# Performance work log

Measured on AMD Instinct MI355X. Metric: run time of the kernel, lower is better.

Reference implementation:

```python
import jax, jax.numpy as jnp
import numpy as np

N, E, D, G, L = 100000, 1600000, 128, 64, 3


def _layernorm(h, g, b, eps=1e-5):
    mu = jnp.mean(h, axis=-1, keepdims=True)
    var = jnp.var(h, axis=-1, keepdims=True)
    return (h - mu) * jax.lax.rsqrt(var + eps) * g + b


def setup_inputs() -> dict:
    key = jax.random.key(0)
    ks = jax.random.split(key, 10)
    s = 1.0 / np.sqrt(D)
    return {
        "x": jax.random.normal(ks[0], (N, D), dtype=jnp.float32),
        "edge_index": jax.random.randint(ks[1], (2, E), 0, N, dtype=jnp.int64),
        "batch": jnp.sort(jax.random.randint(ks[2], (N,), 0, G, dtype=jnp.int64)),
        "fc_w": jax.random.normal(ks[3], (D, D), dtype=jnp.float32) * s,
        "fc_b": jnp.zeros((D,), dtype=jnp.float32),
        "w_self": jax.random.normal(ks[4], (L, D, D), dtype=jnp.float32) * s,
        "w_neigh": jax.random.normal(ks[5], (L, D, D), dtype=jnp.float32) * s,
        "conv_b": jnp.zeros((L, D), dtype=jnp.float32),
        "ln_g": jnp.ones((L, D), dtype=jnp.float32),
        "ln_b": jnp.zeros((L, D), dtype=jnp.float32),
    }


def reference(x, edge_index, batch, fc_w, fc_b, w_self, w_neigh, conv_b, ln_g, ln_b):
    src, dst = edge_index[0], edge_index[1]
    # in-degree for mean aggregation (clamped to avoid div-by-zero)
    deg = jax.ops.segment_sum(jnp.ones((E,), dtype=x.dtype), dst, num_segments=N)
    deg = jnp.maximum(deg, 1.0)[:, None]  # [N,1]

    node = x @ fc_w + fc_b                      # input projection
    graph = jnp.zeros((G, D), dtype=x.dtype)    # initial graph embed (None -> 0)

    for l in range(L):
        # SAGEConv: self transform + mean neighbor aggregation
        agg = jax.ops.segment_sum(node[src], dst, num_segments=N) / deg  # [N,D]
        h = node @ w_self[l] + agg @ w_neigh[l] + conv_b[l]
        g = jax.ops.segment_sum(h, batch, num_segments=G)  # graph_aggr='add'
        # residual (channel_match=True)
        h = h + node
        g = g + graph
        # norm + act (original applies norm twice to graph_out, no relu on it)
        node = jax.nn.relu(_layernorm(h, ln_g[l], ln_b[l]))
        graph = _layernorm(_layernorm(g, ln_g[l], ln_b[l]), ln_g[l], ln_b[l])
    return node, graph
```

## Files before the change

### kernel.cpp

```cpp
#include <hip/hip_runtime.h>

#define D 128
#define NG 64
#define NL 3
#define NPART 8

typedef __attribute__((ext_vector_type(8))) short bf16x8;
typedef __attribute__((ext_vector_type(4))) float f32x4;
typedef unsigned short u16;
typedef unsigned int   u32;

__device__ __forceinline__ u16 f2bf(float x) {
  u32 u = __float_as_uint(x);
  return (u16)((u + 0x7FFF + ((u >> 16) & 1)) >> 16);
}
__device__ __forceinline__ float bf2f(u16 b) {
  return __uint_as_float((u32)b << 16);
}

__global__ void k_count(const int* __restrict__ dst, int* __restrict__ cnt,
                        int E, int psize) {
  const int myp = blockIdx.x & (NPART - 1);
  const int lo  = myp * psize, hi = lo + psize;
  const int tpp = (gridDim.x / NPART) * blockDim.x;
  int i = (blockIdx.x >> 3) * blockDim.x + threadIdx.x;
  for (; i < E; i += tpp) {
    int t = dst[i];
    if (t >= lo && t < hi) atomicAdd(&cnt[t], 1);
  }
}

__global__ void k_fill(const int* __restrict__ src, const int* __restrict__ dst,
                       int* __restrict__ cursor, int* __restrict__ csr_src,
                       int E, int psize) {
  const int myp = blockIdx.x & (NPART - 1);
  const int lo  = myp * psize, hi = lo + psize;
  const int tpp = (gridDim.x / NPART) * blockDim.x;
  int i = (blockIdx.x >> 3) * blockDim.x + threadIdx.x;
  for (; i < E; i += tpp) {
    int t = dst[i];
    int s = src[i];
    if (t >= lo && t < hi) {
      int pos = atomicAdd(&cursor[t], 1);
      csr_src[pos] = s;
    }
  }
}

__global__ void k_invdeg(const int* __restrict__ cnt, float* __restrict__ invdeg, int n) {
  int i = blockIdx.x * blockDim.x + threadIdx.x;
  if (i < n) invdeg[i] = 1.0f / (float)max(cnt[i], 1);
}

__global__ void k_blocksum(const int* __restrict__ cnt, int* __restrict__ bsum, int n) {
  int b = blockIdx.x, t = threadIdx.x;
  int base = b * 1024 + t * 4;
  int s = 0;
#pragma unroll
  for (int j = 0; j < 4; ++j) if (base + j < n) s += cnt[base + j];
  int lane = t & 63, w = t >> 6;
#pragma unroll
  for (int m = 1; m < 64; m <<= 1) s += __shfl_xor(s, m);
  __shared__ int ws[4];
  if (lane == 0) ws[w] = s;
  __syncthreads();
  if (t == 0) bsum[b] = ws[0] + ws[1] + ws[2] + ws[3];
}

__global__ void k_scan_bsum(int* __restrict__ bsum, int nb) {
  __shared__ int s[1024];
  int t = threadIdx.x;
  int v = t < nb ? bsum[t] : 0;
  s[t] = v;
  __syncthreads();
  for (int off = 1; off < 1024; off <<= 1) {
    int x = (t >= off) ? s[t - off] : 0;
    __syncthreads();
    s[t] += x;
    __syncthreads();
  }
  if (t < nb) bsum[t] = s[t] - v;
}

__global__ void k_rowptr(const int* __restrict__ cnt, const int* __restrict__ bsum,
                         int* __restrict__ rowptr, int* __restrict__ cursor, int n) {
  int b = blockIdx.x, t = threadIdx.x;
  int base = b * 1024 + t * 4;
  int v0 = 0, v1 = 0, v2 = 0, v3 = 0;
  if (base + 0 < n) v0 = cnt[base + 0];
  if (base + 1 < n) v1 = cnt[base + 1];
  if (base + 2 < n) v2 = cnt[base + 2];
  if (base + 3 < n) v3 = cnt[base + 3];
  int ts = v0 + v1 + v2 + v3;
  int lane = t & 63, w = t >> 6;
  int incl = ts;
#pragma unroll
  for (int m = 1; m < 64; m <<= 1) {
    int o = __shfl_up(incl, m);
    if (lane >= m) incl += o;
  }
  __shared__ int wsum[4];
  if (lane == 63) wsum[w] = incl;
  __syncthreads();
  int woff = 0;
  for (int i = 0; i < w; ++i) woff += wsum[i];
  int run = incl - ts + woff + bsum[b];
  if (base + 0 < n) { rowptr[base + 0] = run; cursor[base + 0] = run; run += v0; }
  if (base + 1 < n) { rowptr[base + 1] = run; cursor[base + 1] = run; run += v1; }
  if (base + 2 < n) { rowptr[base + 2] = run; cursor[base + 2] = run; run += v2; }
  if (base + 3 < n) { rowptr[base + 3] = run; cursor[base + 3] = run; run += v3; }
}

__global__ void k_wprep(const float* __restrict__ W, u16* __restrict__ Wt, int nmats) {
  long idx = (long)blockIdx.x * blockDim.x + threadIdx.x;
  long total = (long)nmats * 16384;
  long stride = (long)gridDim.x * blockDim.x;
  for (; idx < total; idx += stride) {
    long m = idx >> 14;
    int o = (int)(idx & 16383);
    int nn = o >> 7, k = o & 127;
    Wt[idx] = f2bf(W[m * 16384 + k * 128 + nn]);
  }
}

__global__ void k_aggr(const u16* __restrict__ nodeB,
                       const int* __restrict__ rowptr, const int* __restrict__ rowend,
                       const float* __restrict__ invdeg,
                       const int* __restrict__ csr_src,
                       u16* __restrict__ aggB, int n) {
  const int tid  = threadIdx.x;
  const int lane = tid & 63;
  const int l15  = lane & 15;
  const int g    = lane >> 4;
  const int wav  = (blockIdx.x * blockDim.x + tid) >> 6;
  const int node = wav * 4 + g;
  if (node >= n) return;

  const int s0 = rowptr[node];
  const int nk = rowend[node] - s0;
  const long off = (long)l15 * 8;

  float acc[8] = {};

  for (int kb = 0; kb < nk; kb += 16) {
    const int rem = min(16, nk - kb);
    int myidx = (l15 < rem) ? csr_src[s0 + kb + l15] : 0;
    int kk = 0;
    for (; kk + 8 <= rem; kk += 8) {
      bf16x8 v[8];
#pragma unroll
      for (int j = 0; j < 8; ++j) {
        int s = __shfl(myidx, (g << 4) + kk + j);
        v[j] = *(const bf16x8*)&nodeB[(long)s * D + off];
      }
#pragma unroll
      for (int j = 0; j < 8; ++j)
#pragma unroll
        for (int e = 0; e < 8; ++e)
          acc[e] += bf2f((u16)v[j][e]);
    }
    for (; kk + 4 <= rem; kk += 4) {
      bf16x8 v[4];
#pragma unroll
      for (int j = 0; j < 4; ++j) {
        int s = __shfl(myidx, (g << 4) + kk + j);
        v[j] = *(const bf16x8*)&nodeB[(long)s * D + off];
      }
#pragma unroll
      for (int j = 0; j < 4; ++j)
#pragma unroll
        for (int e = 0; e < 8; ++e)
          acc[e] += bf2f((u16)v[j][e]);
    }
    for (; kk < rem; ++kk) {
      int s = __shfl(myidx, (g << 4) + kk);
      bf16x8 v = *(const bf16x8*)&nodeB[(long)s * D + off];
#pragma unroll
      for (int e = 0; e < 8; ++e) acc[e] += bf2f((u16)v[e]);
    }
  }

  const float sc = invdeg[node];
  bf16x8 ov;
#pragma unroll
  for (int e = 0; e < 8; ++e) ov[e] = (short)f2bf(acc[e] * sc);
  *(bf16x8*)&aggB[(long)node * D + off] = ov;
}

__global__ __launch_bounds__(256) void k_proj_mfma(
    const float* __restrict__ X, const u16* __restrict__ WT,
    const float* __restrict__ bias, u16* __restrict__ OutB, int n)
{
  const int tid  = threadIdx.x;
  const int lane = tid & 63;
  const int w    = tid >> 6;
  const int l15  = lane & 15;
  const int g    = lane >> 4;
  const long base = (long)blockIdx.x * 64;

  long arow  = base + w * 16 + l15;
  long arowc = arow < n ? arow : (n - 1);

  bf16x8 aX[4];
#pragma unroll
  for (int ks = 0; ks < 4; ++ks) {
    int k0 = ks * 32 + g * 8;
    float4 x0 = *(const float4*)&X[arowc * D + k0];
    float4 x1 = *(const float4*)&X[arowc * D + k0 + 4];
    bf16x8 a;
    a[0] = (short)f2bf(x0.x); a[1] = (short)f2bf(x0.y);
    a[2] = (short)f2bf(x0.z); a[3] = (short)f2bf(x0.w);
    a[4] = (short)f2bf(x1.x); a[5] = (short)f2bf(x1.y);
    a[6] = (short)f2bf(x1.z); a[7] = (short)f2bf(x1.w);
    aX[ks] = a;
  }

  f32x4 acc[8] = {};
#pragma unroll
  for (int f = 0; f < 8; ++f) {
    int nn = f * 16 + l15;
#pragma unroll
    for (int ks = 0; ks < 4; ++ks) {
      int k0 = ks * 32 + g * 8;
      bf16x8 bW = *(const bf16x8*)&WT[nn * D + k0];
      acc[f] = __builtin_amdgcn_mfma_f32_16x16x32_bf16(aX[ks], bW, acc[f], 0, 0, 0);
    }
  }

  float bs[8];
#pragma unroll
  for (int f = 0; f < 8; ++f) bs[f] = bias[f * 16 + l15];

#pragma unroll
  for (int r = 0; r < 4; ++r) {
    long row = base + w * 16 + g * 4 + r;
    if (row >= n) continue;
#pragma unroll
    for (int f = 0; f < 8; ++f)
      OutB[row * D + f * 16 + l15] = f2bf(acc[f][r] + bs[f]);
  }
}

__global__ __launch_bounds__(256) void k_conv_mfma(
    const u16* __restrict__ nodeB, const u16* __restrict__ aggB,
    const u16* __restrict__ WsT, const u16* __restrict__ WnT,
    const float* __restrict__ bias,
    const float* __restrict__ lg, const float* __restrict__ lb,
    const int* __restrict__ batch,
    float* __restrict__ gacc,
    u16* __restrict__ nodeOutB, float* __restrict__ nodeOutF,
    int n)
{
  __shared__ int batch_lds[64];
  const int tid  = threadIdx.x;
  const int lane = tid & 63;
  const int w    = tid >> 6;
  const int l15  = lane & 15;
  const int g    = lane >> 4;
  const long base = (long)blockIdx.x * 64;

  if (tid < 64) {
    long r = base + tid;
    batch_lds[tid] = batch[r < n ? r : (n - 1)];
  }
  __syncthreads();

  long arow  = base + w * 16 + l15;
  long arowc = arow < n ? arow : (n - 1);

  bf16x8 aS[4], aA[4];
#pragma unroll
  for (int ks = 0; ks < 4; ++ks) {
    int k0 = ks * 32 + g * 8;
    aS[ks] = *(const bf16x8*)&nodeB[arowc * D + k0];
    aA[ks] = *(const bf16x8*)&aggB [arowc * D + k0];
  }

  f32x4 acc[8] = {};

#pragma unroll
  for (int f = 0; f < 8; ++f) {
    int nn = f * 16 + l15;
#pragma unroll
    for (int ks = 0; ks < 4; ++ks) {
      int k0 = ks * 32 + g * 8;
      bf16x8 bS = *(const bf16x8*)&WsT[nn * D + k0];
      bf16x8 bA = *(const bf16x8*)&WnT[nn * D + k0];
      acc[f] = __builtin_amdgcn_mfma_f32_16x16x32_bf16(aS[ks], bS, acc[f], 0, 0, 0);
      acc[f] = __builtin_amdgcn_mfma_f32_16x16x32_bf16(aA[ks], bA, acc[f], 0, 0, 0);
    }
  }

  float bs[8], lgv[8], lbv[8];
#pragma unroll
  for (int f = 0; f < 8; ++f) {
    bs[f]  = bias[f * 16 + l15];
    lgv[f] = lg[f * 16 + l15];
    lbv[f] = lb[f * 16 + l15];
  }

#pragma unroll
  for (int f = 0; f < 8; ++f)
#pragma unroll
    for (int r = 0; r < 4; ++r) acc[f][r] += bs[f];

  long rowb[4];
  bool valid[4];
#pragma unroll
  for (int r = 0; r < 4; ++r) {
    rowb[r]  = base + w * 16 + g * 4 + r;
    valid[r] = rowb[r] < n;
  }

  const int wb = w * 16;
  int b_first = batch_lds[wb], b_last = batch_lds[wb + 15];
  if (b_first == b_last) {
#pragma unroll
    for (int f = 0; f < 8; ++f) {
      float ps = 0.f;
#pragma unroll
      for (int r = 0; r < 4; ++r) if (valid[r]) ps += acc[f][r];
      ps += __shfl_xor(ps, 16);
      ps += __shfl_xor(ps, 32);
      if (lane < 16) atomicAdd(&gacc[b_first * D + f * 16 + lane], ps);
    }
  } else {
    int i = 0;
    while (i < 16) {
      int bseg = batch_lds[wb + i];
      int j = i + 1;
      while (j < 16 && batch_lds[wb + j] == bseg) ++j;
#pragma unroll
      for (int f = 0; f < 8; ++f) {
        float ps = 0.f;
#pragma unroll
        for (int r = 0; r < 4; ++r) {
          int lr = g * 4 + r;
          if (valid[r] && lr >= i && lr < j) ps += acc[f][r];
        }
        ps += __shfl_xor(ps, 16);
        ps += __shfl_xor(ps, 32);
        if (lane < 16) atomicAdd(&gacc[bseg * D + f * 16 + lane], ps);
      }
      i = j;
    }
  }

  float xv[8][4];
  float s[4] = {0, 0, 0, 0}, q[4] = {0, 0, 0, 0};
#pragma unroll
  for (int r = 0; r < 4; ++r) {
    long row = valid[r] ? rowb[r] : (n - 1);
#pragma unroll
    for (int f = 0; f < 8; ++f) {
      float nv = bf2f(nodeB[row * D + f * 16 + l15]);
      float x  = acc[f][r] + nv;
      xv[f][r] = x;
      s[r] += x; q[r] += x * x;
    }
  }
#pragma unroll
  for (int r = 0; r < 4; ++r) {
#pragma unroll
    for (int m = 1; m < 16; m <<= 1) {
      s[r] += __shfl_xor(s[r], m);
      q[r] += __shfl_xor(q[r], m);
    }
  }
#pragma unroll
  for (int r = 0; r < 4; ++r) {
    if (!valid[r]) continue;
    float mean = s[r] * (1.f / 128.f);
    float var  = q[r] * (1.f / 128.f) - mean * mean;
    float rs   = rsqrtf(fmaxf(var, 0.f) + 1e-5f);
#pragma unroll
    for (int f = 0; f < 8; ++f) {
      float y = fmaxf((xv[f][r] - mean) * rs * lgv[f] + lbv[f], 0.f);
      nodeOutB[rowb[r] * D + f * 16 + l15] = f2bf(y);
      if (nodeOutF) nodeOutF[rowb[r] * D + f * 16 + l15] = y;
    }
  }
}

__global__ void k_ln_graph(const float* __restrict__ gacc,
                           float* __restrict__ graph,
                           const float* __restrict__ lg,
                           const float* __restrict__ lb)
{
  int row  = blockIdx.x;
  int lane = threadIdx.x;
  float2 gv = *(const float2*)&lg[lane * 2];
  float2 bv = *(const float2*)&lb[lane * 2];
  float2 a = *(const float2*)&gacc[row * D + lane * 2];
  float2 p = *(const float2*)&graph[row * D + lane * 2];
  float x0 = a.x + p.x, x1 = a.y + p.y;
#pragma unroll
  for (int pass = 0; pass < 2; ++pass) {
    float s = x0 + x1, q = x0 * x0 + x1 * x1;
#pragma unroll
    for (int m = 1; m < 64; m <<= 1) { s += __shfl_xor(s, m); q += __shfl_xor(q, m); }
    float mean = s * (1.f / 128.f);
    float var  = q * (1.f / 128.f) - mean * mean;
    float rs   = rsqrtf(fmaxf(var, 0.f) + 1e-5f);
    x0 = (x0 - mean) * rs * gv.x + bv.x;
    x1 = (x1 - mean) * rs * gv.y + bv.y;
  }
  float2 o; o.x = x0; o.y = x1;
  *(float2*)&graph[row * D + lane * 2] = o;
}

extern "C" void kernel_launch(void* const* d_in, const int* in_sizes, int n_in,
                              void* d_out, int out_size, void* d_ws, size_t ws_size,
                              hipStream_t stream)
{
  const float* x       = (const float*)d_in[0];
  const int*   edge    = (const int*)d_in[1];
  const int*   batch   = (const int*)d_in[2];
  const float* fc_w    = (const float*)d_in[3];
  const float* fc_b    = (const float*)d_in[4];
  const float* w_self  = (const float*)d_in[5];
  const float* w_neigh = (const float*)d_in[6];
  const float* conv_b  = (const float*)d_in[7];
  const float* ln_g    = (const float*)d_in[8];
  const float* ln_b    = (const float*)d_in[9];

  const int N = in_sizes[0] / D;
  const int E = in_sizes[1] / 2;
  const int* src = edge;
  const int* dst = edge + E;

  int*   cnt      = (int*)d_ws;
  int*   rowptr   = cnt + N;
  int*   cursor   = rowptr + N;
  int*   bsum     = cursor + N;
  int*   csr_src  = bsum + 1024;
  float* invdeg   = (float*)(csr_src + E);
  float* gacc     = invdeg + N;
  float* graphbuf = gacc + NG * D;
  char*  bfbase   = (char*)(graphbuf + NG * D);
  bfbase = (char*)(((size_t)bfbase + 15) & ~(size_t)15);
  u16*   nodeB    = (u16*)bfbase;
  u16*   aggB     = nodeB + (long)N * D;
  u16*   wsT      = aggB + (long)N * D;
  u16*   wnT      = wsT + 3 * D * D;
  u16*   fcT      = wnT + 3 * D * D;

  const int nb = (N + 1023) / 1024;
  const int psize = (N + NPART - 1) / NPART;

  hipMemsetAsync(cnt, 0, (size_t)N * sizeof(int), stream);
  hipMemsetAsync(graphbuf, 0, (size_t)NG * D * sizeof(float), stream);

  k_count<<<2048, 256, 0, stream>>>(dst, cnt, E, psize);
  k_invdeg<<<(N + 255) / 256, 256, 0, stream>>>(cnt, invdeg, N);
  k_blocksum<<<nb, 256, 0, stream>>>(cnt, bsum, N);
  k_scan_bsum<<<1, 1024, 0, stream>>>(bsum, nb);
  k_rowptr<<<nb, 256, 0, stream>>>(cnt, bsum, rowptr, cursor, N);
  k_fill<<<2048, 256, 0, stream>>>(src, dst, cursor, csr_src, E, psize);

  k_wprep<<<192, 256, 0, stream>>>(w_self,  wsT, NL);
  k_wprep<<<192, 256, 0, stream>>>(w_neigh, wnT, NL);
  k_wprep<<<64, 256, 0, stream>>>(fc_w, fcT, 1);

  const int cblocks = (N + 63) / 64;
  k_proj_mfma<<<cblocks, 256, 0, stream>>>(x, fcT, fc_b, nodeB, N);

  const int ablocks = (N + 15) / 16;
  for (int l = 0; l < NL; ++l) {
    hipMemsetAsync(gacc, 0, (size_t)NG * D * sizeof(float), stream);
    k_aggr<<<ablocks, 256, 0, stream>>>(nodeB, rowptr, cursor, invdeg,
                                        csr_src, aggB, N);
    k_conv_mfma<<<cblocks, 256, 0, stream>>>(
        nodeB, aggB, wsT + (long)l * D * D, wnT + (long)l * D * D,
        conv_b + l * D, ln_g + l * D, ln_b + l * D,
        batch, gacc,
        nodeB, (l == NL - 1) ? (float*)d_out : nullptr, N);
    k_ln_graph<<<NG, 64, 0, stream>>>(gacc, graphbuf, ln_g + l * D, ln_b + l * D);
  }

  hipMemcpyAsync((float*)d_out + (long)N * D, graphbuf,
                 (size_t)NG * D * sizeof(float),
                 hipMemcpyDeviceToDevice, stream);
}
```

Baseline: 587.7 us.

## Stage MFMA results through LDS for row-contiguous epilogue and column-wise graph reduction

```diff
diff --git a/kernel.cpp b/kernel.cpp
--- a/kernel.cpp
+++ b/kernel.cpp
@@ -191,6 +191,7 @@
     const float* __restrict__ X, const u16* __restrict__ WT,
     const float* __restrict__ bias, u16* __restrict__ OutB, int n)
 {
+  __shared__ float h_lds[64][132];
   const int tid  = threadIdx.x;
   const int lane = tid & 63;
   const int w    = tid >> 6;
@@ -227,17 +228,34 @@
     }
   }
 
-  float bs[8];
-#pragma unroll
-  for (int f = 0; f < 8; ++f) bs[f] = bias[f * 16 + l15];
-
-#pragma unroll
-  for (int r = 0; r < 4; ++r) {
-    long row = base + w * 16 + g * 4 + r;
-    if (row >= n) continue;
-#pragma unroll
-    for (int f = 0; f < 8; ++f)
-      OutB[row * D + f * 16 + l15] = f2bf(acc[f][r] + bs[f]);
+#pragma unroll
+  for (int f = 0; f < 8; ++f)
+#pragma unroll
+    for (int r = 0; r < 4; ++r)
+      h_lds[w * 16 + g * 4 + r][f * 16 + l15] = acc[f][r];
+  __syncthreads();
+
+  const int row = tid >> 2;
+  const int q   = tid & 3;
+  const long grow = base + row;
+  if (grow < n) {
+    bf16x8 ov[4];
+#pragma unroll
+    for (int i = 0; i < 4; ++i) {
+      float4 h0 = *(const float4*)&h_lds[row][q * 32 + i * 8];
+      float4 h1 = *(const float4*)&h_lds[row][q * 32 + i * 8 + 4];
+      float4 b0 = *(const float4*)&bias[q * 32 + i * 8];
+      float4 b1 = *(const float4*)&bias[q * 32 + i * 8 + 4];
+      bf16x8 o;
+      o[0] = (short)f2bf(h0.x + b0.x); o[1] = (short)f2bf(h0.y + b0.y);
+      o[2] = (short)f2bf(h0.z + b0.z); o[3] = (short)f2bf(h0.w + b0.w);
+      o[4] = (short)f2bf(h1.x + b1.x); o[5] = (short)f2bf(h1.y + b1.y);
+      o[6] = (short)f2bf(h1.z + b1.z); o[7] = (short)f2bf(h1.w + b1.w);
+      ov[i] = o;
+    }
+#pragma unroll
+    for (int i = 0; i < 4; ++i)
+      *(bf16x8*)&OutB[grow * D + q * 32 + i * 8] = ov[i];
   }
 }
 
@@ -251,6 +269,7 @@
     u16* __restrict__ nodeOutB, float* __restrict__ nodeOutF,
     int n)
 {
+  __shared__ float h_lds[64][132];
   __shared__ int batch_lds[64];
   const int tid  = threadIdx.x;
   const int lane = tid & 63;
@@ -263,7 +282,6 @@
     long r = base + tid;
     batch_lds[tid] = batch[r < n ? r : (n - 1)];
   }
-  __syncthreads();
 
   long arow  = base + w * 16 + l15;
   long arowc = arow < n ? arow : (n - 1);
@@ -277,7 +295,6 @@
   }
 
   f32x4 acc[8] = {};
-
 #pragma unroll
   for (int f = 0; f < 8; ++f) {
     int nn = f * 16 + l15;
@@ -291,93 +308,76 @@
     }
   }
 
-  float bs[8], lgv[8], lbv[8];
-#pragma unroll
-  for (int f = 0; f < 8; ++f) {
-    bs[f]  = bias[f * 16 + l15];
-    lgv[f] = lg[f * 16 + l15];
-    lbv[f] = lb[f * 16 + l15];
-  }
-
+  float bs[8];
+#pragma unroll
+  for (int f = 0; f < 8; ++f) bs[f] = bias[f * 16 + l15];
 #pragma unroll
   for (int f = 0; f < 8; ++f)
 #pragma unroll
-    for (int r = 0; r < 4; ++r) acc[f][r] += bs[f];
-
-  long rowb[4];
-  bool valid[4];
-#pragma unroll
-  for (int r = 0; r < 4; ++r) {
-    rowb[r]  = base + w * 16 + g * 4 + r;
-    valid[r] = rowb[r] < n;
-  }
-
-  const int wb = w * 16;
-  int b_first = batch_lds[wb], b_last = batch_lds[wb + 15];
-  if (b_first == b_last) {
-#pragma unroll
-    for (int f = 0; f < 8; ++f) {
-      float ps = 0.f;
-#pragma unroll
-      for (int r = 0; r < 4; ++r) if (valid[r]) ps += acc[f][r];
-      ps += __shfl_xor(ps, 16);
-      ps += __shfl_xor(ps, 32);
-      if (lane < 16) atomicAdd(&gacc[b_first * D + f * 16 + lane], ps);
-    }
-  } else {
-    int i = 0;
-    while (i < 16) {
-      int bseg = batch_lds[wb + i];
-      int j = i + 1;
-      while (j < 16 && batch_lds[wb + j] == bseg) ++j;
-#pragma unroll
-      for (int f = 0; f < 8; ++f) {
-        float ps = 0.f;
-#pragma unroll
-        for (int r = 0; r < 4; ++r) {
-          int lr = g * 4 + r;
-          if (valid[r] && lr >= i && lr < j) ps += acc[f][r];
-        }
-        ps += __shfl_xor(ps, 16);
-        ps += __shfl_xor(ps, 32);
-        if (lane < 16) atomicAdd(&gacc[bseg * D + f * 16 + lane], ps);
+    for (int r = 0; r < 4; ++r)
+      h_lds[w * 16 + g * 4 + r][f * 16 + l15] = acc[f][r] + bs[f];
+  __syncthreads();
+
+  const long nrem = n - base;
+  const int rmax = nrem > 64 ? 64 : (int)nrem;
+
+  if (tid < 128) {
+    const int c = tid;
+    float s = 0.f;
+    int cur = batch_lds[0];
+    for (int r = 0; r < rmax; ++r) {
+      int b = batch_lds[r];
+      if (b != cur) { atomicAdd(&gacc[cur * D + c], s); s = 0.f; cur = b; }
+      s += h_lds[r][c];
+    }
+    atomicAdd(&gacc[cur * D + c], s);
+  }
+
+  const int row = tid >> 2;
+  const int q   = tid & 3;
+  if (row < rmax) {
+    const long grow = base + row;
+    float h[32];
+    float s = 0.f, qs = 0.f;
+#pragma unroll
+    for (int i = 0; i < 4; ++i) {
+      float4 h0 = *(const float4*)&h_lds[row][q * 32 + i * 8];
+      float4 h1 = *(const float4*)&h_lds[row][q * 32 + i * 8 + 4];
+      bf16x8 nv = *(const bf16x8*)&nodeB[grow * D + q * 32 + i * 8];
+      h[i*8+0] = h0.x + bf2f((u16)nv[0]); h[i*8+1] = h0.y + bf2f((u16)nv[1]);
+      h[i*8+2] = h0.z + bf2f((u16)nv[2]); h[i*8+3] = h0.w + bf2f((u16)nv[3]);
+      h[i*8+4] = h1.x + bf2f((u16)nv[4]); h[i*8+5] = h1.y + bf2f((u16)nv[5]);
+      h[i*8+6] = h1.z + bf2f((u16)nv[6]); h[i*8+7] = h1.w + bf2f((u16)nv[7]);
+#pragma unroll
+      for (int e = 0; e < 8; ++e) { s += h[i*8+e]; qs += h[i*8+e] * h[i*8+e]; }
+    }
+    s  += __shfl_xor(s, 1);  s  += __shfl_xor(s, 2);
+    qs += __shfl_xor(qs, 1); qs += __shfl_xor(qs, 2);
+    float mean = s * (1.f / 128.f);
+    float var  = qs * (1.f / 128.f) - mean * mean;
+    float rs   = rsqrtf(fmaxf(var, 0.f) + 1e-5f);
+#pragma unroll
+    for (int i = 0; i < 8; ++i) {
+      float4 gv = *(const float4*)&lg[q * 32 + i * 4];
+      float4 bv = *(const float4*)&lb[q * 32 + i * 4];
+      h[i*4+0] = fmaxf((h[i*4+0] - mean) * rs * gv.x + bv.x, 0.f);
+      h[i*4+1] = fmaxf((h[i*4+1] - mean) * rs * gv.y + bv.y, 0.f);
+      h[i*4+2] = fmaxf((h[i*4+2] - mean) * rs * gv.z + bv.z, 0.f);
+      h[i*4+3] = fmaxf((h[i*4+3] - mean) * rs * gv.w + bv.w, 0.f);
+    }
+    if (nodeOutB) {
+#pragma unroll
+      for (int i = 0; i < 4; ++i) {
+        bf16x8 o;
+#pragma unroll
+        for (int e = 0; e < 8; ++e) o[e] = (short)f2bf(h[i*8+e]);
+        *(bf16x8*)&nodeOutB[grow * D + q * 32 + i * 8] = o;
       }
-      i = j;
-    }
-  }
-
-  float xv[8][4];
-  float s[4] = {0, 0, 0, 0}, q[4] = {0, 0, 0, 0};
-#pragma unroll
-  for (int r = 0; r < 4; ++r) {
-    long row = valid[r] ? rowb[r] : (n - 1);
-#pragma unroll
-    for (int f = 0; f < 8; ++f) {
-      float nv = bf2f(nodeB[row * D + f * 16 + l15]);
-      float x  = acc[f][r] + nv;
-      xv[f][r] = x;
-      s[r] += x; q[r] += x * x;
-    }
-  }
-#pragma unroll
-  for (int r = 0; r < 4; ++r) {
-#pragma unroll
-    for (int m = 1; m < 16; m <<= 1) {
-      s[r] += __shfl_xor(s[r], m);
-      q[r] += __shfl_xor(q[r], m);
-    }
-  }
-#pragma unroll
-  for (int r = 0; r < 4; ++r) {
-    if (!valid[r]) continue;
-    float mean = s[r] * (1.f / 128.f);
-    float var  = q[r] * (1.f / 128.f) - mean * mean;
-    float rs   = rsqrtf(fmaxf(var, 0.f) + 1e-5f);
-#pragma unroll
-    for (int f = 0; f < 8; ++f) {
-      float y = fmaxf((xv[f][r] - mean) * rs * lgv[f] + lbv[f], 0.f);
-      nodeOutB[rowb[r] * D + f * 16 + l15] = f2bf(y);
-      if (nodeOutF) nodeOutF[rowb[r] * D + f * 16 + l15] = y;
+    }
+    if (nodeOutF) {
+#pragma unroll
+      for (int i = 0; i < 8; ++i)
+        *(float4*)&nodeOutF[grow * D + q * 32 + i * 4] = *(const float4*)&h[i*4];
     }
   }
 }
@@ -470,11 +470,12 @@
     hipMemsetAsync(gacc, 0, (size_t)NG * D * sizeof(float), stream);
     k_aggr<<<ablocks, 256, 0, stream>>>(nodeB, rowptr, cursor, invdeg,
                                         csr_src, aggB, N);
+    const bool last = (l == NL - 1);
     k_conv_mfma<<<cblocks, 256, 0, stream>>>(
         nodeB, aggB, wsT + (long)l * D * D, wnT + (long)l * D * D,
         conv_b + l * D, ln_g + l * D, ln_b + l * D,
         batch, gacc,
-        nodeB, (l == NL - 1) ? (float*)d_out : nullptr, N);
+        last ? nullptr : nodeB, last ? (float*)d_out : nullptr, N);
     k_ln_graph<<<NG, 64, 0, stream>>>(gacc, graphbuf, ln_g + l * D, ln_b + l * D);
   }
 
```

Result: slower. 634.4 us (+7.9%).
